# Optimization experiments

Measured on AMD Instinct MI355X. Metric: run time of the kernel, lower is better.

## Reference

```python
import jax, jax.numpy as jnp
import numpy as np

B, S1, S2 = 4, 2048, 2048
IN1, IN2 = 512, 512
KD, VD, H = 64, 64, 8


def setup_inputs() -> dict:
    key = jax.random.key(0)
    ks = jax.random.split(key, 7)
    x1 = jax.random.normal(ks[0], (B, S1, IN1), dtype=jnp.float32)
    x2 = jax.random.normal(ks[1], (B, S2, IN2), dtype=jnp.float32)
    # nn.Linear weights stored as [out, in]; kaiming-uniform-ish scale
    Wq = jax.random.normal(ks[2], (KD * H, IN1), dtype=jnp.float32) * (1.0 / np.sqrt(IN1))
    Wk = jax.random.normal(ks[3], (KD * H, IN2), dtype=jnp.float32) * (1.0 / np.sqrt(IN2))
    Wv = jax.random.normal(ks[4], (VD * H, IN2), dtype=jnp.float32) * (1.0 / np.sqrt(IN2))
    Wo = jax.random.normal(ks[5], (IN1, VD * H), dtype=jnp.float32) * (1.0 / np.sqrt(VD * H))
    bo = jax.random.normal(ks[6], (IN1,), dtype=jnp.float32) * 0.01
    return {"x1": x1, "x2": x2, "Wq": Wq, "Wk": Wk, "Wv": Wv, "Wo": Wo, "bo": bo}


def reference(x1, x2, Wq, Wk, Wv, Wo, bo):
    b, s1, _ = x1.shape
    s2 = x2.shape[1]
    # projections -> [B, H, S, D]
    q = (x1 @ Wq.T).reshape(b, s1, H, KD).transpose(0, 2, 1, 3)
    k = (x2 @ Wk.T).reshape(b, s2, H, KD).transpose(0, 2, 1, 3)
    v = (x2 @ Wv.T).reshape(b, s2, H, VD).transpose(0, 2, 1, 3)
    # scores [B, H, S1, S2]
    attn = jnp.einsum('bhqd,bhkd->bhqk', q, k) / jnp.sqrt(jnp.float32(KD))
    attn = jax.nn.softmax(attn, axis=-1)
    out = jnp.einsum('bhqk,bhkd->bhqd', attn, v)  # [B, H, S1, VD]
    out = out.transpose(0, 2, 1, 3).reshape(b, s1, H * VD)
    return out @ Wo.T + bo
```

## Files before the change

kernel.cpp:

```cpp
#include <hip/hip_runtime.h>
#include <stdint.h>

typedef __bf16 bf16;
typedef __bf16 bf16x8 __attribute__((ext_vector_type(8)));
typedef __bf16 bf16x4 __attribute__((ext_vector_type(4)));
typedef float f32x4 __attribute__((ext_vector_type(4)));

#define MFMA16x16x32(A, B, C) __builtin_amdgcn_mfma_f32_16x16x32_bf16((A), (B), (C), 0, 0, 0)

__device__ __forceinline__ void gload_lds16(const void* g, void* l) {
  __builtin_amdgcn_global_load_lds((const __attribute__((address_space(1))) void*)g,
                                   (__attribute__((address_space(3))) void*)l,
                                   16, 0, 0);
}

__device__ __forceinline__ float fexp2(float x) { return __builtin_amdgcn_exp2f(x); }

__global__ void cvt_f32_to_bf16(const float* __restrict__ in, bf16* __restrict__ out, int n) {
  int i = (blockIdx.x * blockDim.x + threadIdx.x) * 4;
  if (i >= n) return;
  float4 v = *reinterpret_cast<const float4*>(in + i);
  bf16x4 o;
  o[0] = (bf16)v.x; o[1] = (bf16)v.y; o[2] = (bf16)v.z; o[3] = (bf16)v.w;
  *reinterpret_cast<bf16x4*>(out + i) = o;
}

__global__ void cvt_w4(const float* __restrict__ w0, const float* __restrict__ w1,
                       const float* __restrict__ w2, const float* __restrict__ w3,
                       bf16* __restrict__ out) {
  const int y = blockIdx.y;
  const float* src = (y == 0) ? w0 : (y == 1) ? w1 : (y == 2) ? w2 : w3;
  int i = (blockIdx.x * blockDim.x + threadIdx.x) * 4;
  float4 v = *reinterpret_cast<const float4*>(src + i);
  bf16x4 o;
  o[0] = (bf16)v.x; o[1] = (bf16)v.y; o[2] = (bf16)v.z; o[3] = (bf16)v.w;
  *reinterpret_cast<bf16x4*>(out + (size_t)y * 262144 + i) = o;
}

template <int MODE>
__global__ __launch_bounds__(256, 2) void gemm_bt_kernel(
    const bf16* __restrict__ A, const bf16* __restrict__ B,
    void* __restrict__ C, const float* __restrict__ bias,
    int N, int K, float scale) {
  __shared__ bf16 As[2][128 * 32];
  __shared__ bf16 Bs[2][64 * 32];
  const int tid = threadIdx.x;
  const int w = tid >> 6, l = tid & 63;
  const int wr = w >> 1, wc = w & 1;
  const int lr = l & 15, lg = l >> 4;
  const int bm = blockIdx.x, bn = blockIdx.y;

  const bf16* Ab = A + (size_t)bm * 128 * K;
  const bf16* Bb = B + (size_t)bn * 64 * K;

  const int c_row = l >> 2;
  const int c_col = ((l & 3) ^ (c_row & 3)) * 8;

  auto stage = [&](int k0, int bb) {
#pragma unroll
    for (int i = 0; i < 2; i++) {
      const int q = w + i * 4;
      gload_lds16(Ab + (size_t)(q * 16 + c_row) * K + k0 + c_col, &As[bb][q * 512]);
    }
    gload_lds16(Bb + (size_t)(w * 16 + c_row) * K + k0 + c_col, &Bs[bb][w * 512]);
  };

  f32x4 acc[4][2] = {};
  const int swz = (lr & 3) * 8;

  stage(0, 0);
  stage(32, 1);

  const int NT = K / 32;
  for (int t = 0; t < NT; t++) {
    if (t == NT - 1) asm volatile("s_waitcnt vmcnt(0)" ::: "memory");
    else             asm volatile("s_waitcnt vmcnt(3)" ::: "memory");
    __syncthreads();
    const int cur = t & 1;
    bf16x8 a[4], b[2];
#pragma unroll
    for (int mi = 0; mi < 4; mi++)
      a[mi] = *reinterpret_cast<const bf16x8*>(
          &As[cur][(wr * 64 + mi * 16 + lr) * 32 + (lg * 8 ^ swz)]);
#pragma unroll
    for (int ni = 0; ni < 2; ni++)
      b[ni] = *reinterpret_cast<const bf16x8*>(
          &Bs[cur][(wc * 32 + ni * 16 + lr) * 32 + (lg * 8 ^ swz)]);
#pragma unroll
    for (int mi = 0; mi < 4; mi++)
#pragma unroll
      for (int ni = 0; ni < 2; ni++)
        acc[mi][ni] = MFMA16x16x32(a[mi], b[ni], acc[mi][ni]);
    __syncthreads();
    if (t + 2 < NT) stage((t + 2) * 32, cur);
  }

#pragma unroll
  for (int mi = 0; mi < 4; mi++) {
    const int m0 = bm * 128 + wr * 64 + mi * 16 + lg * 4;
#pragma unroll
    for (int ni = 0; ni < 2; ni++) {
      const int n = bn * 64 + wc * 32 + ni * 16 + lr;
#pragma unroll
      for (int r = 0; r < 4; r++) {
        const int m = m0 + r;
        float v = acc[mi][ni][r];
        if constexpr (MODE == 0) {
          v *= scale;
          size_t d = (size_t)((m >> 11) * 8 + (n >> 6)) * 131072 + (size_t)(m & 2047) * 64 + (n & 63);
          ((bf16*)C)[d] = (bf16)v;
        } else if constexpr (MODE == 1) {
          size_t d = ((size_t)(n >> 11) * 512 + m) * 2048 + (n & 2047);
          ((bf16*)C)[d] = (bf16)v;
        } else {
          ((float*)C)[(size_t)m * N + n] = v + bias[n];
        }
      }
    }
  }
}

__global__ __launch_bounds__(512, 1) void attn_kernel(
    const bf16* __restrict__ Q, const bf16* __restrict__ Kk,
    const bf16* __restrict__ Vt, bf16* __restrict__ AO) {
  __shared__ bf16 Kb2[2][64 * 64];
  __shared__ bf16 Vb2[2][64 * 64];
  __shared__ bf16 Ps[8][32 * 64];

  const int tid = threadIdx.x;
  const int w = tid >> 6, l = tid & 63;
  const int lr = l & 15, lg = l >> 4;

  const int lin = blockIdx.x;
  const int xcd = lin & 7;
  const int m = lin >> 3;
  const int bh = xcd * 4 + (m & 3);
  const int qb = m >> 2;
  const int b = bh >> 3, h = bh & 7;

  const bf16* Qb = Q + (size_t)bh * 131072;
  const bf16* Kb = Kk + (size_t)bh * 131072;
  const bf16* Vb = Vt + (size_t)bh * 131072;

  const int q0 = qb * 256 + w * 32;

  bf16x8 qf[2][2];
#pragma unroll
  for (int i = 0; i < 2; i++)
#pragma unroll
    for (int ks = 0; ks < 2; ks++)
      qf[i][ks] = *reinterpret_cast<const bf16x8*>(
          Qb + (size_t)(q0 + i * 16 + lr) * 64 + ks * 32 + lg * 8);

  const int crow = l >> 3;
  const int scol = ((l & 7) ^ crow) * 8;

  auto stage = [&](int kv0, int bb) {
    const int row = w * 8 + crow;
    gload_lds16(Kb + (size_t)(kv0 + row) * 64 + scol, &Kb2[bb][w * 512]);
    gload_lds16(Vb + (size_t)row * 2048 + kv0 + scol, &Vb2[bb][w * 512]);
  };

  f32x4 oacc[2][4] = {};
  float lsum[2] = {0.f, 0.f};
  const int sw8 = (lr & 7) * 8;

  stage(0, 0);
  stage(64, 1);

  for (int t = 0; t < 32; t++) {
    if (t == 31) asm volatile("s_waitcnt vmcnt(0)" ::: "memory");
    else         asm volatile("s_waitcnt vmcnt(2)" ::: "memory");
    __syncthreads();
    const int cur = t & 1;

    bf16x8 kb[2][4];
#pragma unroll
    for (int ks = 0; ks < 2; ks++)
#pragma unroll
      for (int c = 0; c < 4; c++)
        kb[ks][c] = *reinterpret_cast<const bf16x8*>(
            &Kb2[cur][(c * 16 + lr) * 64 + ((ks * 32 + lg * 8) ^ sw8)]);

#pragma unroll
    for (int i = 0; i < 2; i++) {
      f32x4 st[4] = {};
#pragma unroll
      for (int ks = 0; ks < 2; ks++)
#pragma unroll
        for (int c = 0; c < 4; c++)
          st[c] = MFMA16x16x32(kb[ks][c], qf[i][ks], st[c]);
#pragma unroll
      for (int c = 0; c < 4; c++) {
        float e0 = fexp2(st[c][0]);
        float e1 = fexp2(st[c][1]);
        float e2 = fexp2(st[c][2]);
        float e3 = fexp2(st[c][3]);
        lsum[i] += (e0 + e1) + (e2 + e3);
        bf16x4 pk;
        pk[0] = (bf16)e0; pk[1] = (bf16)e1; pk[2] = (bf16)e2; pk[3] = (bf16)e3;
        *reinterpret_cast<bf16x4*>(
            &Ps[w][(i * 16 + lr) * 64 + ((c * 16 + lg * 4) ^ sw8)]) = pk;
      }
    }

    bf16x8 vb[2][4];
#pragma unroll
    for (int ks = 0; ks < 2; ks++)
#pragma unroll
      for (int c = 0; c < 4; c++)
        vb[ks][c] = *reinterpret_cast<const bf16x8*>(
            &Vb2[cur][(c * 16 + lr) * 64 + ((ks * 32 + lg * 8) ^ sw8)]);

#pragma unroll
    for (int i = 0; i < 2; i++)
#pragma unroll
      for (int ks = 0; ks < 2; ks++) {
        bf16x8 pa = *reinterpret_cast<const bf16x8*>(
            &Ps[w][(i * 16 + lr) * 64 + ((ks * 32 + lg * 8) ^ sw8)]);
#pragma unroll
        for (int c = 0; c < 4; c++)
          oacc[i][c] = MFMA16x16x32(pa, vb[ks][c], oacc[i][c]);
      }

    __syncthreads();
    if (t + 2 < 32) stage((t + 2) * 64, cur);
  }

#pragma unroll
  for (int i = 0; i < 2; i++) {
    lsum[i] += __shfl_xor(lsum[i], 16);
    lsum[i] += __shfl_xor(lsum[i], 32);
  }

#pragma unroll
  for (int i = 0; i < 2; i++) {
#pragma unroll
    for (int r = 0; r < 4; r++) {
      const float inv = 1.f / __shfl(lsum[i], lg * 4 + r);
      const int qrow = q0 + i * 16 + lg * 4 + r;
#pragma unroll
      for (int c = 0; c < 4; c++)
        AO[(size_t)(b * 2048 + qrow) * 512 + h * 64 + c * 16 + lr] = (bf16)(oacc[i][c][r] * inv);
    }
  }
}

extern "C" void kernel_launch(void* const* d_in, const int* in_sizes, int n_in,
                              void* d_out, int out_size, void* d_ws, size_t ws_size,
                              hipStream_t stream) {
  (void)in_sizes; (void)n_in; (void)out_size; (void)ws_size;
  const float* x1 = (const float*)d_in[0];
  const float* x2 = (const float*)d_in[1];
  const float* Wq = (const float*)d_in[2];
  const float* Wk = (const float*)d_in[3];
  const float* Wv = (const float*)d_in[4];
  const float* Wo = (const float*)d_in[5];
  const float* bo = (const float*)d_in[6];

  uint8_t* ws = (uint8_t*)d_ws;
  bf16* x1b = (bf16*)(ws + 0);
  bf16* AO  = (bf16*)(ws + 0);
  bf16* x2b = (bf16*)(ws + 8388608);
  bf16* Wqb = (bf16*)(ws + 16777216);
  bf16* Wkb = (bf16*)(ws + 17301504);
  bf16* Wvb = (bf16*)(ws + 17825792);
  bf16* Wob = (bf16*)(ws + 18350080);
  bf16* Qws = (bf16*)(ws + 18874368);
  bf16* Kws = (bf16*)(ws + 27262976);
  bf16* Vtw = (bf16*)(ws + 35651584);

  const int n_x = 4 * 2048 * 512;

  cvt_f32_to_bf16<<<n_x / 1024, 256, 0, stream>>>(x1, x1b, n_x);
  cvt_f32_to_bf16<<<n_x / 1024, 256, 0, stream>>>(x2, x2b, n_x);
  cvt_w4<<<dim3(256, 4), 256, 0, stream>>>(Wq, Wk, Wv, Wo, Wqb);

  gemm_bt_kernel<0><<<dim3(64, 8), 256, 0, stream>>>(x1b, Wqb, Qws, nullptr, 512, 512, 0.18033688011112f);
  gemm_bt_kernel<0><<<dim3(64, 8), 256, 0, stream>>>(x2b, Wkb, Kws, nullptr, 512, 512, 1.0f);
  gemm_bt_kernel<1><<<dim3(4, 128), 256, 0, stream>>>(Wvb, x2b, Vtw, nullptr, 8192, 512, 1.0f);

  attn_kernel<<<256, 512, 0, stream>>>(Qws, Kws, Vtw, AO);

  gemm_bt_kernel<2><<<dim3(64, 8), 256, 0, stream>>>(AO, Wob, d_out, bo, 512, 512, 1.0f);
}
```

Baseline: 111.4 us.

## Fuse fp32-to-bf16 conversion into projection GEMMs and merge K/V projections

Removes the separate conversion kernels by having the projection GEMMs load fp32 activations and weights into registers and convert them to bf16 on the way into LDS. K and V projections now share one launch over x2, and the V output is written transposed with vector stores. The GEMM and attention pipelines are restructured from two-stage async global-to-LDS prefetch to a single-stage prefetch with a full vmcnt(0) wait each iteration. This cuts launches and the intermediate bf16 traffic, but doubles global read bytes for the fp32 operands and weakens the latency hiding in attention and the GEMMs.

Measured after the change: 155.5 us. 1.4x slower.

```diff
diff --git a/kernel.cpp b/kernel.cpp
--- a/kernel.cpp
+++ b/kernel.cpp
@@ -16,32 +16,18 @@
 
 __device__ __forceinline__ float fexp2(float x) { return __builtin_amdgcn_exp2f(x); }
 
-__global__ void cvt_f32_to_bf16(const float* __restrict__ in, bf16* __restrict__ out, int n) {
-  int i = (blockIdx.x * blockDim.x + threadIdx.x) * 4;
-  if (i >= n) return;
-  float4 v = *reinterpret_cast<const float4*>(in + i);
-  bf16x4 o;
-  o[0] = (bf16)v.x; o[1] = (bf16)v.y; o[2] = (bf16)v.z; o[3] = (bf16)v.w;
-  *reinterpret_cast<bf16x4*>(out + i) = o;
-}
-
-__global__ void cvt_w4(const float* __restrict__ w0, const float* __restrict__ w1,
-                       const float* __restrict__ w2, const float* __restrict__ w3,
-                       bf16* __restrict__ out) {
-  const int y = blockIdx.y;
-  const float* src = (y == 0) ? w0 : (y == 1) ? w1 : (y == 2) ? w2 : w3;
-  int i = (blockIdx.x * blockDim.x + threadIdx.x) * 4;
-  float4 v = *reinterpret_cast<const float4*>(src + i);
-  bf16x4 o;
-  o[0] = (bf16)v.x; o[1] = (bf16)v.y; o[2] = (bf16)v.z; o[3] = (bf16)v.w;
-  *reinterpret_cast<bf16x4*>(out + (size_t)y * 262144 + i) = o;
+__device__ __forceinline__ bf16x8 cvt8(float4 a, float4 b) {
+  bf16x8 o;
+  o[0] = (bf16)a.x; o[1] = (bf16)a.y; o[2] = (bf16)a.z; o[3] = (bf16)a.w;
+  o[4] = (bf16)b.x; o[5] = (bf16)b.y; o[6] = (bf16)b.z; o[7] = (bf16)b.w;
+  return o;
 }
 
 template <int MODE>
-__global__ __launch_bounds__(256, 2) void gemm_bt_kernel(
-    const bf16* __restrict__ A, const bf16* __restrict__ B,
-    void* __restrict__ C, const float* __restrict__ bias,
-    int N, int K, float scale) {
+__global__ __launch_bounds__(256, 2) void proj_kernel(
+    const void* __restrict__ Aptr, const float* __restrict__ B0f,
+    const float* __restrict__ B1f, void* __restrict__ C0,
+    void* __restrict__ C1, const float* __restrict__ bias, float scale) {
   __shared__ bf16 As[2][128 * 32];
   __shared__ bf16 Bs[2][64 * 32];
   const int tid = threadIdx.x;
@@ -49,34 +35,63 @@
   const int wr = w >> 1, wc = w & 1;
   const int lr = l & 15, lg = l >> 4;
   const int bm = blockIdx.x, bn = blockIdx.y;
-
-  const bf16* Ab = A + (size_t)bm * 128 * K;
-  const bf16* Bb = B + (size_t)bn * 64 * K;
+  const int K = 512;
+
+  const float* Bf = (MODE == 1 && bn >= 8) ? B1f + (size_t)(bn - 8) * 64 * K
+                                           : B0f + (size_t)bn * 64 * K;
+  const float* Af32 = (const float*)Aptr;
+  const bf16* Abf = (const bf16*)Aptr;
 
   const int c_row = l >> 2;
-  const int c_col = ((l & 3) ^ (c_row & 3)) * 8;
-
-  auto stage = [&](int k0, int bb) {
-#pragma unroll
-    for (int i = 0; i < 2; i++) {
-      const int q = w + i * 4;
-      gload_lds16(Ab + (size_t)(q * 16 + c_row) * K + k0 + c_col, &As[bb][q * 512]);
-    }
-    gload_lds16(Bb + (size_t)(w * 16 + c_row) * K + k0 + c_col, &Bs[bb][w * 512]);
+  const int c_s = l & 3;
+  const int sw = (c_s ^ (c_row & 3)) * 8;
+
+  float4 la[2][2], lb[2];
+
+  auto issue = [&](int t, int bb) {
+    const int k0 = t * 32;
+    if constexpr (MODE == 2) {
+#pragma unroll
+      for (int i = 0; i < 2; i++) {
+        const int q = w + i * 4;
+        gload_lds16(Abf + (size_t)(bm * 128 + q * 16 + c_row) * K + k0 + sw, &As[bb][q * 512]);
+      }
+    } else {
+#pragma unroll
+      for (int i = 0; i < 2; i++) {
+        const int q = w + i * 4;
+        const float* p = Af32 + (size_t)(bm * 128 + q * 16 + c_row) * K + k0 + c_s * 8;
+        la[i][0] = *reinterpret_cast<const float4*>(p);
+        la[i][1] = *reinterpret_cast<const float4*>(p + 4);
+      }
+    }
+    const float* pb = Bf + (size_t)(w * 16 + c_row) * K + k0 + c_s * 8;
+    lb[0] = *reinterpret_cast<const float4*>(pb);
+    lb[1] = *reinterpret_cast<const float4*>(pb + 4);
+  };
+  auto commit = [&](int bb) {
+    if constexpr (MODE != 2) {
+#pragma unroll
+      for (int i = 0; i < 2; i++) {
+        const int q = w + i * 4;
+        *reinterpret_cast<bf16x8*>(&As[bb][q * 512 + c_row * 32 + sw]) = cvt8(la[i][0], la[i][1]);
+      }
+    }
+    *reinterpret_cast<bf16x8*>(&Bs[bb][w * 512 + c_row * 32 + sw]) = cvt8(lb[0], lb[1]);
   };
 
   f32x4 acc[4][2] = {};
   const int swz = (lr & 3) * 8;
 
-  stage(0, 0);
-  stage(32, 1);
-
+  issue(0, 0);
+  asm volatile("s_waitcnt vmcnt(0)" ::: "memory");
+  commit(0);
+  __syncthreads();
+
+  int cur = 0;
   const int NT = K / 32;
   for (int t = 0; t < NT; t++) {
-    if (t == NT - 1) asm volatile("s_waitcnt vmcnt(0)" ::: "memory");
-    else             asm volatile("s_waitcnt vmcnt(3)" ::: "memory");
-    __syncthreads();
-    const int cur = t & 1;
+    if (t + 1 < NT) issue(t + 1, cur ^ 1);
     bf16x8 a[4], b[2];
 #pragma unroll
     for (int mi = 0; mi < 4; mi++)
@@ -91,8 +106,12 @@
 #pragma unroll
       for (int ni = 0; ni < 2; ni++)
         acc[mi][ni] = MFMA16x16x32(a[mi], b[ni], acc[mi][ni]);
+    if (t + 1 < NT) {
+      asm volatile("s_waitcnt vmcnt(0)" ::: "memory");
+      commit(cur ^ 1);
+    }
     __syncthreads();
-    if (t + 2 < NT) stage((t + 2) * 32, cur);
+    cur ^= 1;
   }
 
 #pragma unroll
@@ -100,21 +119,37 @@
     const int m0 = bm * 128 + wr * 64 + mi * 16 + lg * 4;
 #pragma unroll
     for (int ni = 0; ni < 2; ni++) {
-      const int n = bn * 64 + wc * 32 + ni * 16 + lr;
-#pragma unroll
-      for (int r = 0; r < 4; r++) {
-        const int m = m0 + r;
-        float v = acc[mi][ni][r];
-        if constexpr (MODE == 0) {
-          v *= scale;
-          size_t d = (size_t)((m >> 11) * 8 + (n >> 6)) * 131072 + (size_t)(m & 2047) * 64 + (n & 63);
-          ((bf16*)C)[d] = (bf16)v;
-        } else if constexpr (MODE == 1) {
-          size_t d = ((size_t)(n >> 11) * 512 + m) * 2048 + (n & 2047);
-          ((bf16*)C)[d] = (bf16)v;
+      const int n = wc * 32 + ni * 16 + lr;
+      if constexpr (MODE == 0) {
+#pragma unroll
+        for (int r = 0; r < 4; r++) {
+          const int m = m0 + r, gn = bn * 64 + n;
+          float v = acc[mi][ni][r] * scale;
+          size_t d = (size_t)((m >> 11) * 8 + (gn >> 6)) * 131072 + (size_t)(m & 2047) * 64 + (gn & 63);
+          ((bf16*)C0)[d] = (bf16)v;
+        }
+      } else if constexpr (MODE == 1) {
+        if (bn < 8) {
+#pragma unroll
+          for (int r = 0; r < 4; r++) {
+            const int m = m0 + r, gn = bn * 64 + n;
+            size_t d = (size_t)((m >> 11) * 8 + (gn >> 6)) * 131072 + (size_t)(m & 2047) * 64 + (gn & 63);
+            ((bf16*)C0)[d] = (bf16)acc[mi][ni][r];
+          }
         } else {
-          ((float*)C)[(size_t)m * N + n] = v + bias[n];
+          const int nv = (bn - 8) * 64 + n;
+          bf16x4 pv;
+#pragma unroll
+          for (int r = 0; r < 4; r++) pv[r] = (bf16)acc[mi][ni][r];
+          size_t base = ((size_t)(m0 >> 11) * 512 + nv) * 2048 + (m0 & 2047);
+          *reinterpret_cast<bf16x4*>((bf16*)C1 + base) = pv;
         }
+      } else {
+        const int gn = bn * 64 + n;
+        const float bv = bias[gn];
+#pragma unroll
+        for (int r = 0; r < 4; r++)
+          ((float*)C0)[(size_t)(m0 + r) * 512 + gn] = acc[mi][ni][r] + bv;
       }
     }
   }
@@ -166,13 +201,12 @@
   const int sw8 = (lr & 7) * 8;
 
   stage(0, 0);
-  stage(64, 1);
+  asm volatile("s_waitcnt vmcnt(0)" ::: "memory");
+  __syncthreads();
 
   for (int t = 0; t < 32; t++) {
-    if (t == 31) asm volatile("s_waitcnt vmcnt(0)" ::: "memory");
-    else         asm volatile("s_waitcnt vmcnt(2)" ::: "memory");
-    __syncthreads();
     const int cur = t & 1;
+    if (t < 31) stage((t + 1) * 64, cur ^ 1);
 
     bf16x8 kb[2][4];
 #pragma unroll
@@ -223,8 +257,8 @@
           oacc[i][c] = MFMA16x16x32(pa, vb[ks][c], oacc[i][c]);
       }
 
+    if (t < 31) asm volatile("s_waitcnt vmcnt(0)" ::: "memory");
     __syncthreads();
-    if (t + 2 < 32) stage((t + 2) * 64, cur);
   }
 
 #pragma unroll
@@ -259,28 +293,15 @@
   const float* bo = (const float*)d_in[6];
 
   uint8_t* ws = (uint8_t*)d_ws;
-  bf16* x1b = (bf16*)(ws + 0);
-  bf16* AO  = (bf16*)(ws + 0);
-  bf16* x2b = (bf16*)(ws + 8388608);
-  bf16* Wqb = (bf16*)(ws + 16777216);
-  bf16* Wkb = (bf16*)(ws + 17301504);
-  bf16* Wvb = (bf16*)(ws + 17825792);
-  bf16* Wob = (bf16*)(ws + 18350080);
-  bf16* Qws = (bf16*)(ws + 18874368);
-  bf16* Kws = (bf16*)(ws + 27262976);
-  bf16* Vtw = (bf16*)(ws + 35651584);
-
-  const int n_x = 4 * 2048 * 512;
-
-  cvt_f32_to_bf16<<<n_x / 1024, 256, 0, stream>>>(x1, x1b, n_x);
-  cvt_f32_to_bf16<<<n_x / 1024, 256, 0, stream>>>(x2, x2b, n_x);
-  cvt_w4<<<dim3(256, 4), 256, 0, stream>>>(Wq, Wk, Wv, Wo, Wqb);
-
-  gemm_bt_kernel<0><<<dim3(64, 8), 256, 0, stream>>>(x1b, Wqb, Qws, nullptr, 512, 512, 0.18033688011112f);
-  gemm_bt_kernel<0><<<dim3(64, 8), 256, 0, stream>>>(x2b, Wkb, Kws, nullptr, 512, 512, 1.0f);
-  gemm_bt_kernel<1><<<dim3(4, 128), 256, 0, stream>>>(Wvb, x2b, Vtw, nullptr, 8192, 512, 1.0f);
+  bf16* Qws = (bf16*)(ws + 0);
+  bf16* Kws = (bf16*)(ws + 8388608);
+  bf16* Vtw = (bf16*)(ws + 16777216);
+  bf16* AO  = (bf16*)(ws + 25165824);
+
+  proj_kernel<0><<<dim3(64, 8), 256, 0, stream>>>(x1, Wq, nullptr, Qws, nullptr, nullptr, 0.18033688011112f);
+  proj_kernel<1><<<dim3(64, 16), 256, 0, stream>>>(x2, Wk, Wv, Kws, Vtw, nullptr, 1.0f);
 
   attn_kernel<<<256, 512, 0, stream>>>(Qws, Kws, Vtw, AO);
 
-  gemm_bt_kernel<2><<<dim3(64, 8), 256, 0, stream>>>(AO, Wob, d_out, bo, 512, 512, 1.0f);
-}
+  proj_kernel<2><<<dim3(64, 8), 256, 0, stream>>>(AO, Wo, nullptr, d_out, nullptr, bo, 1.0f);
+}
```
